# Optimization experiments

Measured on AMD Instinct MI355X. Metric: run time of the kernel, lower is better.

Reference implementation:

```python
import jax, jax.numpy as jnp
import numpy as np

B, N, C, DK, TOPK = 4, 4096, 256, 64, 8


def setup_inputs() -> dict:
    key = jax.random.key(0)
    k1, k2, k3 = jax.random.split(key, 3)
    x = jax.random.normal(k1, (B, N, C), dtype=jnp.float32)
    # nn.Linear(channels, d_k, bias=False) weights, stored as [C, DK] for x @ W
    W_q = jax.random.normal(k2, (C, DK), dtype=jnp.float32) * (C ** -0.5)
    W_k = jax.random.normal(k3, (C, DK), dtype=jnp.float32) * (C ** -0.5)
    return {"x": x, "W_q": W_q, "W_k": W_k, "top_k": TOPK}


def reference(x, W_q, W_k, top_k):
    d_k = W_q.shape[-1]
    scale = d_k ** -0.5
    Q = x @ W_q                                   # [B, N, DK]
    K = x @ W_k                                   # [B, N, DK]
    S = jnp.einsum('bnd,bmd->bnm', Q, K) * scale  # [B, N, N]
    _, topk_idx = jax.lax.top_k(S, top_k)         # [B, N, top_k]
    n = S.shape[-1]
    # scatter True at top-k column indices per row (mirrors torch scatter_)
    row_mask = lambda idx: jnp.zeros((n,), dtype=bool).at[idx].set(True)
    mask = jax.vmap(jax.vmap(row_mask))(topk_idx)  # [B, N, N] bool
    S_masked = jnp.where(mask, S, -jnp.inf)
    A = jax.nn.softmax(S_masked, axis=-1)
    return A
```

## Files before the change

kernel.cpp:

```cpp
#include <hip/hip_runtime.h>
#include <math.h>

#define NROW 16384
#define NCOL 4096
#define CDIM 256
#define DKDIM 64
#define SCALE 0.125f

typedef float v4f __attribute__((ext_vector_type(4)));

__global__ __launch_bounds__(512, 2) void qk_proj(
    const float* __restrict__ x, const float* __restrict__ Wq,
    const float* __restrict__ Wk, float* __restrict__ Qt,
    float* __restrict__ Kt) {
  __shared__ float4 xs4[64][65];
  const int t = threadIdx.x;
  const int rb = blockIdx.x;
  {
    const float4* xg = (const float4*)(x + (size_t)rb * 64 * CDIM);
    #pragma unroll
    for (int i = 0; i < 8; ++i) {
      int idx = i * 512 + t;
      xs4[idx >> 6][idx & 63] = xg[idx];
    }
  }
  __syncthreads();

  const int lane = t & 63;
  const int wu = __builtin_amdgcn_readfirstlane(t >> 6);
  const int proj = wu >> 2;
  const int chunk = wu & 3;
  const float* __restrict__ Wp = proj ? Wk : Wq;

  float acc[16];
  #pragma unroll
  for (int j = 0; j < 16; ++j) acc[j] = 0.f;

  #pragma unroll 4
  for (int cs = 0; cs < 64; ++cs) {
    float4 xv = xs4[lane][cs];
    const float xc[4] = {xv.x, xv.y, xv.z, xv.w};
    #pragma unroll
    for (int i = 0; i < 4; ++i) {
      const float4* __restrict__ w4 =
          (const float4*)(Wp + (size_t)(cs * 4 + i) * DKDIM + chunk * 16);
      float4 wa = w4[0], wb = w4[1], wc = w4[2], wd = w4[3];
      float xi = xc[i];
      acc[0]  = fmaf(xi, wa.x, acc[0]);  acc[1]  = fmaf(xi, wa.y, acc[1]);
      acc[2]  = fmaf(xi, wa.z, acc[2]);  acc[3]  = fmaf(xi, wa.w, acc[3]);
      acc[4]  = fmaf(xi, wb.x, acc[4]);  acc[5]  = fmaf(xi, wb.y, acc[5]);
      acc[6]  = fmaf(xi, wb.z, acc[6]);  acc[7]  = fmaf(xi, wb.w, acc[7]);
      acc[8]  = fmaf(xi, wc.x, acc[8]);  acc[9]  = fmaf(xi, wc.y, acc[9]);
      acc[10] = fmaf(xi, wc.z, acc[10]); acc[11] = fmaf(xi, wc.w, acc[11]);
      acc[12] = fmaf(xi, wd.x, acc[12]); acc[13] = fmaf(xi, wd.y, acc[13]);
      acc[14] = fmaf(xi, wd.z, acc[14]); acc[15] = fmaf(xi, wd.w, acc[15]);
    }
  }

  const int gr = rb * 64 + lane;
  const int b = gr >> 12;
  const int n = gr & 4095;
  float4* __restrict__ Out4 = (float4*)(proj ? Kt : Qt);
  #pragma unroll
  for (int i = 0; i < 4; ++i) {
    int dg = chunk * 4 + i;
    float4 o = {acc[4 * i], acc[4 * i + 1], acc[4 * i + 2], acc[4 * i + 3]};
    Out4[(size_t)(b * 16 + dg) * 4096 + n] = o;
  }
}

__global__ __launch_bounds__(256, 8) void s_topk(
    const float* __restrict__ Qt, const float* __restrict__ Kt,
    float* __restrict__ out, float* __restrict__ wsv, int* __restrict__ wsi) {
  __shared__ float smem[4224];
  float4* qs = (float4*)smem;
  float (*cv)[33] = (float(*)[33])smem;
  int   (*ci)[33] = (int(*)[33])(smem + 64 * 33);

  const int t = threadIdx.x;
  const int f = blockIdx.x;
  const int xs = f & 7;
  const int i5 = f >> 3;
  const int combo = xs * 4 + (i5 >> 6);
  const int rbL = i5 & 63;
  const int b = combo >> 3;
  const int chunk = combo & 7;
  const int rb = b * 64 + rbL;
  const int lane = t & 63;
  const int wu = __builtin_amdgcn_readfirstlane(t >> 6);
  const int nb = rbL * 64;

  const float4* __restrict__ Qt4 = (const float4*)Qt;
  #pragma unroll
  for (int i = 0; i < 4; ++i) {
    int idx = i * 256 + t;
    int g = idx >> 6, row = idx & 63;
    qs[g * 64 + row] = Qt4[(size_t)(b * 16 + g) * 4096 + nb + row];
  }
  __syncthreads();

  {
    v4f z = {0.f, 0.f, 0.f, 0.f};
    v4f* o4 = (v4f*)out + (size_t)rb * 64 * 1024 + chunk * 128;
    #pragma unroll 8
    for (int i = 0; i < 32; ++i) {
      int g = i * 256 + t;
      __builtin_nontemporal_store(z, &o4[(size_t)(g >> 7) * 1024 + (g & 127)]);
    }
  }

  const float4* __restrict__ Kt4 = (const float4*)Kt;
  const int stripe = chunk * 512 + wu * 128;

  float tv[8]; int ti[8]; float tmin; int tmpos;

  auto compute8 = [&](int cb, float* acc) {
    #pragma unroll
    for (int j = 0; j < 8; ++j) acc[j] = 0.f;
    #pragma unroll 2
    for (int g = 0; g < 16; ++g) {
      float4 qf = qs[g * 64 + lane];
      const float4* __restrict__ kg =
          Kt4 + (size_t)(b * 16 + g) * 4096 + cb;
      #pragma unroll
      for (int j = 0; j < 8; ++j) {
        float4 kf = kg[j];
        acc[j] = fmaf(qf.x, kf.x, acc[j]);
        acc[j] = fmaf(qf.y, kf.y, acc[j]);
        acc[j] = fmaf(qf.z, kf.z, acc[j]);
        acc[j] = fmaf(qf.w, kf.w, acc[j]);
      }
    }
  };

  {
    float acc[8];
    compute8(stripe, acc);
    #pragma unroll
    for (int j = 0; j < 8; ++j) { tv[j] = acc[j]; ti[j] = stripe + j; }
    tmin = tv[0]; tmpos = 0;
    #pragma unroll
    for (int q2 = 1; q2 < 8; ++q2)
      if (tv[q2] < tmin) { tmin = tv[q2]; tmpos = q2; }
  }

  #pragma unroll 1
  for (int cg = 1; cg < 16; ++cg) {
    const int cb = stripe + cg * 8;
    float acc[8];
    compute8(cb, acc);

    float bv = acc[0]; int bj = 0;
    #pragma unroll
    for (int j = 1; j < 8; ++j)
      if (acc[j] > bv) { bv = acc[j]; bj = j; }

    #pragma unroll
    for (int pass = 0; pass < 2; ++pass) {
      if (__any(bv > tmin)) {
        if (bv > tmin) {
          int col = cb + bj;
          #pragma unroll
          for (int q2 = 0; q2 < 8; ++q2)
            if (q2 == tmpos) { tv[q2] = bv; ti[q2] = col; }
          tmin = tv[0]; tmpos = 0;
          #pragma unroll
          for (int q2 = 1; q2 < 8; ++q2)
            if (tv[q2] < tmin) { tmin = tv[q2]; tmpos = q2; }
          #pragma unroll
          for (int j = 0; j < 8; ++j)
            if (j == bj) acc[j] = -INFINITY;
        }
        bv = acc[0]; bj = 0;
        #pragma unroll
        for (int j = 1; j < 8; ++j)
          if (acc[j] > bv) { bv = acc[j]; bj = j; }
      }
    }
    if (__any(bv > tmin)) {
      #pragma unroll
      for (int j = 0; j < 8; ++j) {
        float v = acc[j];
        if (v > tmin) {
          int col = cb + j;
          #pragma unroll
          for (int q2 = 0; q2 < 8; ++q2)
            if (q2 == tmpos) { tv[q2] = v; ti[q2] = col; }
          tmin = tv[0]; tmpos = 0;
          #pragma unroll
          for (int q2 = 1; q2 < 8; ++q2)
            if (tv[q2] < tmin) { tmin = tv[q2]; tmpos = q2; }
        }
      }
    }
  }

  __syncthreads();
  #pragma unroll
  for (int q2 = 0; q2 < 8; ++q2) {
    cv[lane][wu * 8 + q2] = tv[q2];
    ci[lane][wu * 8 + q2] = ti[q2];
  }
  __syncthreads();
  if (t < 64) {
    float rv[8]; int rid[8];
    #pragma unroll
    for (int q2 = 0; q2 < 8; ++q2) { rv[q2] = cv[t][q2]; rid[q2] = ci[t][q2]; }
    float m = rv[0]; int mp = 0;
    #pragma unroll
    for (int q2 = 1; q2 < 8; ++q2) if (rv[q2] < m) { m = rv[q2]; mp = q2; }
    #pragma unroll
    for (int c = 8; c < 32; ++c) {
      float v = cv[t][c];
      if (v > m) {
        int col = ci[t][c];
        #pragma unroll
        for (int q2 = 0; q2 < 8; ++q2) if (q2 == mp) { rv[q2] = v; rid[q2] = col; }
        m = rv[0]; mp = 0;
        #pragma unroll
        for (int q2 = 1; q2 < 8; ++q2) if (rv[q2] < m) { m = rv[q2]; mp = q2; }
      }
    }
    size_t gr = (size_t)rb * 64 + t;
    #pragma unroll
    for (int q2 = 0; q2 < 8; ++q2) {
      wsv[gr * 64 + chunk * 8 + q2] = rv[q2];
      wsi[gr * 64 + chunk * 8 + q2] = rid[q2];
    }
  }
}

__global__ __launch_bounds__(256) void merge_scatter(
    const float* __restrict__ wsv, const int* __restrict__ wsi,
    float* __restrict__ out) {
  int row = blockIdx.x * 256 + threadIdx.x;
  const float4* v4 = (const float4*)(wsv + (size_t)row * 64);
  const int4*   i4 = (const int4*)(wsi + (size_t)row * 64);
  float rv[8]; int rid[8];
  {
    float4 a0 = v4[0], a1 = v4[1];
    int4   c0 = i4[0], c1 = i4[1];
    rv[0]=a0.x; rv[1]=a0.y; rv[2]=a0.z; rv[3]=a0.w;
    rv[4]=a1.x; rv[5]=a1.y; rv[6]=a1.z; rv[7]=a1.w;
    rid[0]=c0.x; rid[1]=c0.y; rid[2]=c0.z; rid[3]=c0.w;
    rid[4]=c1.x; rid[5]=c1.y; rid[6]=c1.z; rid[7]=c1.w;
  }
  float m = rv[0]; int mp = 0;
  #pragma unroll
  for (int q = 1; q < 8; ++q) if (rv[q] < m) { m = rv[q]; mp = q; }
  #pragma unroll 2
  for (int c4 = 2; c4 < 16; ++c4) {
    float4 a = v4[c4]; int4 ic = i4[c4];
    const float vv[4] = {a.x, a.y, a.z, a.w};
    const int   ii[4] = {ic.x, ic.y, ic.z, ic.w};
    #pragma unroll
    for (int k = 0; k < 4; ++k) {
      if (vv[k] > m) {
        #pragma unroll
        for (int q = 0; q < 8; ++q) if (q == mp) { rv[q] = vv[k]; rid[q] = ii[k]; }
        m = rv[0]; mp = 0;
        #pragma unroll
        for (int q = 1; q < 8; ++q) if (rv[q] < m) { m = rv[q]; mp = q; }
      }
    }
  }
  float vmax = rv[0];
  #pragma unroll
  for (int q = 1; q < 8; ++q) vmax = fmaxf(vmax, rv[q]);
  float e[8], s = 0.f;
  #pragma unroll
  for (int q = 0; q < 8; ++q) { e[q] = __expf((rv[q] - vmax) * SCALE); s += e[q]; }
  float inv = 1.f / s;
  float* orow = out + (size_t)row * NCOL;
  #pragma unroll
  for (int q = 0; q < 8; ++q) orow[rid[q]] = e[q] * inv;
}

extern "C" void kernel_launch(void* const* d_in, const int* in_sizes, int n_in,
                              void* d_out, int out_size, void* d_ws, size_t ws_size,
                              hipStream_t stream) {
  const float* x  = (const float*)d_in[0];
  const float* Wq = (const float*)d_in[1];
  const float* Wk = (const float*)d_in[2];
  float* out = (float*)d_out;

  char* ws = (char*)d_ws;
  float* Qt  = (float*)ws;
  float* Kt  = (float*)(ws + (size_t)NROW * DKDIM * 4);
  float* wsv = (float*)(ws + 2 * (size_t)NROW * DKDIM * 4);
  int*   wsi = (int*)  (ws + 2 * (size_t)NROW * DKDIM * 4 + (size_t)NROW * 64 * 4);

  qk_proj<<<dim3(NROW / 64), 512, 0, stream>>>(x, Wq, Wk, Qt, Kt);
  s_topk<<<2048, 256, 0, stream>>>(Qt, Kt, out, wsv, wsi);
  merge_scatter<<<NROW / 256, 256, 0, stream>>>(wsv, wsi, out);
}
```

Baseline: 537.5 us.

## Process two query rows per lane in s_topk to reuse K loads

Each block now handles 128 query rows instead of 64, so every lane computes scores for two rows against the same loaded K vectors and keeps two independent top-8 lists. This halves the global/L2 K traffic per score and doubles FMA work per load. In exchange it uses more registers (launch bounds lowered to 4 blocks/CU), doubles shared memory, and halves the grid to 1024 blocks, which lowers occupancy and parallelism.

```diff
diff --git a/kernel.cpp b/kernel.cpp
--- a/kernel.cpp
+++ b/kernel.cpp
@@ -69,41 +69,41 @@
   }
 }
 
-__global__ __launch_bounds__(256, 8) void s_topk(
+__global__ __launch_bounds__(256, 4) void s_topk(
     const float* __restrict__ Qt, const float* __restrict__ Kt,
     float* __restrict__ out, float* __restrict__ wsv, int* __restrict__ wsi) {
-  __shared__ float smem[4224];
+  __shared__ float smem[8448];
   float4* qs = (float4*)smem;
   float (*cv)[33] = (float(*)[33])smem;
-  int   (*ci)[33] = (int(*)[33])(smem + 64 * 33);
+  int   (*ci)[33] = (int(*)[33])(smem + 128 * 33);
 
   const int t = threadIdx.x;
   const int f = blockIdx.x;
-  const int xs = f & 7;
+  const int slot = f & 7;
   const int i5 = f >> 3;
-  const int combo = xs * 4 + (i5 >> 6);
-  const int rbL = i5 & 63;
+  const int cl = i5 >> 5;
+  const int rbL = i5 & 31;
+  const int combo = slot * 4 + cl;
   const int b = combo >> 3;
   const int chunk = combo & 7;
-  const int rb = b * 64 + rbL;
   const int lane = t & 63;
   const int wu = __builtin_amdgcn_readfirstlane(t >> 6);
-  const int nb = rbL * 64;
+  const int n0 = rbL * 128;
 
   const float4* __restrict__ Qt4 = (const float4*)Qt;
   #pragma unroll
-  for (int i = 0; i < 4; ++i) {
+  for (int i = 0; i < 8; ++i) {
     int idx = i * 256 + t;
-    int g = idx >> 6, row = idx & 63;
-    qs[g * 64 + row] = Qt4[(size_t)(b * 16 + g) * 4096 + nb + row];
+    int g = idx >> 7, row = idx & 127;
+    qs[g * 128 + row] = Qt4[(size_t)(b * 16 + g) * 4096 + n0 + row];
   }
   __syncthreads();
 
   {
     v4f z = {0.f, 0.f, 0.f, 0.f};
-    v4f* o4 = (v4f*)out + (size_t)rb * 64 * 1024 + chunk * 128;
+    v4f* o4 = (v4f*)out + (size_t)(b * 4096 + n0) * 1024 + chunk * 128;
     #pragma unroll 8
-    for (int i = 0; i < 32; ++i) {
+    for (int i = 0; i < 64; ++i) {
       int g = i * 256 + t;
       __builtin_nontemporal_store(z, &o4[(size_t)(g >> 7) * 1024 + (g & 127)]);
     }
@@ -112,49 +112,39 @@
   const float4* __restrict__ Kt4 = (const float4*)Kt;
   const int stripe = chunk * 512 + wu * 128;
 
-  float tv[8]; int ti[8]; float tmin; int tmpos;
-
-  auto compute8 = [&](int cb, float* acc) {
-    #pragma unroll
-    for (int j = 0; j < 8; ++j) acc[j] = 0.f;
+  float tv0[8], tv1[8]; int ti0[8], ti1[8];
+  float tmin0, tmin1; int tmpos0, tmpos1;
+
+  auto compute8 = [&](int cb, float* a0, float* a1) {
+    #pragma unroll
+    for (int j = 0; j < 8; ++j) { a0[j] = 0.f; a1[j] = 0.f; }
     #pragma unroll 2
     for (int g = 0; g < 16; ++g) {
-      float4 qf = qs[g * 64 + lane];
+      float4 qa = qs[g * 128 + lane];
+      float4 qb = qs[g * 128 + 64 + lane];
       const float4* __restrict__ kg =
           Kt4 + (size_t)(b * 16 + g) * 4096 + cb;
       #pragma unroll
       for (int j = 0; j < 8; ++j) {
         float4 kf = kg[j];
-        acc[j] = fmaf(qf.x, kf.x, acc[j]);
-        acc[j] = fmaf(qf.y, kf.y, acc[j]);
-        acc[j] = fmaf(qf.z, kf.z, acc[j]);
-        acc[j] = fmaf(qf.w, kf.w, acc[j]);
+        a0[j] = fmaf(qa.x, kf.x, a0[j]);
+        a0[j] = fmaf(qa.y, kf.y, a0[j]);
+        a0[j] = fmaf(qa.z, kf.z, a0[j]);
+        a0[j] = fmaf(qa.w, kf.w, a0[j]);
+        a1[j] = fmaf(qb.x, kf.x, a1[j]);
+        a1[j] = fmaf(qb.y, kf.y, a1[j]);
+        a1[j] = fmaf(qb.z, kf.z, a1[j]);
+        a1[j] = fmaf(qb.w, kf.w, a1[j]);
       }
     }
   };
 
-  {
-    float acc[8];
-    compute8(stripe, acc);
-    #pragma unroll
-    for (int j = 0; j < 8; ++j) { tv[j] = acc[j]; ti[j] = stripe + j; }
-    tmin = tv[0]; tmpos = 0;
-    #pragma unroll
-    for (int q2 = 1; q2 < 8; ++q2)
-      if (tv[q2] < tmin) { tmin = tv[q2]; tmpos = q2; }
-  }
-
-  #pragma unroll 1
-  for (int cg = 1; cg < 16; ++cg) {
-    const int cb = stripe + cg * 8;
-    float acc[8];
-    compute8(cb, acc);
-
+  auto update8 = [&](int cb, float* acc, float* tv, int* ti,
+                     float& tmin, int& tmpos) {
     float bv = acc[0]; int bj = 0;
     #pragma unroll
     for (int j = 1; j < 8; ++j)
       if (acc[j] > bv) { bv = acc[j]; bj = j; }
-
     #pragma unroll
     for (int pass = 0; pass < 2; ++pass) {
       if (__any(bv > tmin)) {
@@ -193,16 +183,41 @@
         }
       }
     }
+  };
+
+  {
+    float a0[8], a1[8];
+    compute8(stripe, a0, a1);
+    #pragma unroll
+    for (int j = 0; j < 8; ++j) {
+      tv0[j] = a0[j]; ti0[j] = stripe + j;
+      tv1[j] = a1[j]; ti1[j] = stripe + j;
+    }
+    tmin0 = tv0[0]; tmpos0 = 0; tmin1 = tv1[0]; tmpos1 = 0;
+    #pragma unroll
+    for (int q2 = 1; q2 < 8; ++q2) {
+      if (tv0[q2] < tmin0) { tmin0 = tv0[q2]; tmpos0 = q2; }
+      if (tv1[q2] < tmin1) { tmin1 = tv1[q2]; tmpos1 = q2; }
+    }
+  }
+
+  #pragma unroll 1
+  for (int cg = 1; cg < 16; ++cg) {
+    const int cb = stripe + cg * 8;
+    float a0[8], a1[8];
+    compute8(cb, a0, a1);
+    update8(cb, a0, tv0, ti0, tmin0, tmpos0);
+    update8(cb, a1, tv1, ti1, tmin1, tmpos1);
   }
 
   __syncthreads();
   #pragma unroll
   for (int q2 = 0; q2 < 8; ++q2) {
-    cv[lane][wu * 8 + q2] = tv[q2];
-    ci[lane][wu * 8 + q2] = ti[q2];
+    cv[lane][wu * 8 + q2] = tv0[q2];       ci[lane][wu * 8 + q2] = ti0[q2];
+    cv[lane + 64][wu * 8 + q2] = tv1[q2];  ci[lane + 64][wu * 8 + q2] = ti1[q2];
   }
   __syncthreads();
-  if (t < 64) {
+  if (t < 128) {
     float rv[8]; int rid[8];
     #pragma unroll
     for (int q2 = 0; q2 < 8; ++q2) { rv[q2] = cv[t][q2]; rid[q2] = ci[t][q2]; }
@@ -221,7 +236,7 @@
         for (int q2 = 1; q2 < 8; ++q2) if (rv[q2] < m) { m = rv[q2]; mp = q2; }
       }
     }
-    size_t gr = (size_t)rb * 64 + t;
+    size_t gr = (size_t)(b * 4096 + n0) + t;
     #pragma unroll
     for (int q2 = 0; q2 < 8; ++q2) {
       wsv[gr * 64 + chunk * 8 + q2] = rv[q2];
@@ -291,6 +306,6 @@
   int*   wsi = (int*)  (ws + 2 * (size_t)NROW * DKDIM * 4 + (size_t)NROW * 64 * 4);
 
   qk_proj<<<dim3(NROW / 64), 512, 0, stream>>>(x, Wq, Wk, Qt, Kt);
-  s_topk<<<2048, 256, 0, stream>>>(Qt, Kt, out, wsv, wsi);
+  s_topk<<<1024, 256, 0, stream>>>(Qt, Kt, out, wsv, wsi);
   merge_scatter<<<NROW / 256, 256, 0, stream>>>(wsv, wsi, out);
 }
```

New measurement: 546.8 us. No clear change (+1.7%).

## Tile K layout into 8-column blocks, software-pipeline K loads, defer zero-fill stores

Applied to the files above, without the earlier changes.

The K projection is now written in a blocked layout: for each group of 8 columns, all 16 d-groups of 8 float4s sit contiguously, so each column-group's K tile is one 2KB contiguous read. The score loop is hand-unrolled with double-buffered register loads, so the next d-group loads while the current one's FMAs run. The zero-fill of the output is moved after the top-k search so stores no longer compete with the K loads. The top-k initialization is unified via -inf, and launch bounds are relaxed to 4 blocks per SM to allow more registers, at the cost of occupancy.

```diff
diff --git a/kernel.cpp b/kernel.cpp
--- a/kernel.cpp
+++ b/kernel.cpp
@@ -60,16 +60,26 @@
   const int gr = rb * 64 + lane;
   const int b = gr >> 12;
   const int n = gr & 4095;
-  float4* __restrict__ Out4 = (float4*)(proj ? Kt : Qt);
-  #pragma unroll
-  for (int i = 0; i < 4; ++i) {
-    int dg = chunk * 4 + i;
-    float4 o = {acc[4 * i], acc[4 * i + 1], acc[4 * i + 2], acc[4 * i + 3]};
-    Out4[(size_t)(b * 16 + dg) * 4096 + n] = o;
+  if (proj == 0) {
+    float4* __restrict__ Out4 = (float4*)Qt;
+    #pragma unroll
+    for (int i = 0; i < 4; ++i) {
+      int dg = chunk * 4 + i;
+      float4 o = {acc[4 * i], acc[4 * i + 1], acc[4 * i + 2], acc[4 * i + 3]};
+      Out4[(size_t)(b * 16 + dg) * 4096 + n] = o;
+    }
+  } else {
+    float4* __restrict__ Out4 = (float4*)Kt;
+    #pragma unroll
+    for (int i = 0; i < 4; ++i) {
+      int dg = chunk * 4 + i;
+      float4 o = {acc[4 * i], acc[4 * i + 1], acc[4 * i + 2], acc[4 * i + 3]};
+      Out4[(((size_t)b * 512 + (n >> 3)) * 16 + dg) * 8 + (n & 7)] = o;
+    }
   }
 }
 
-__global__ __launch_bounds__(256, 8) void s_topk(
+__global__ __launch_bounds__(256, 4) void s_topk(
     const float* __restrict__ Qt, const float* __restrict__ Kt,
     float* __restrict__ out, float* __restrict__ wsv, int* __restrict__ wsi) {
   __shared__ float smem[4224];
@@ -79,9 +89,9 @@
 
   const int t = threadIdx.x;
   const int f = blockIdx.x;
-  const int xs = f & 7;
+  const int slot = f & 7;
   const int i5 = f >> 3;
-  const int combo = xs * 4 + (i5 >> 6);
+  const int combo = slot * 4 + (i5 >> 6);
   const int rbL = i5 & 63;
   const int b = combo >> 3;
   const int chunk = combo & 7;
@@ -99,62 +109,66 @@
   }
   __syncthreads();
 
-  {
-    v4f z = {0.f, 0.f, 0.f, 0.f};
-    v4f* o4 = (v4f*)out + (size_t)rb * 64 * 1024 + chunk * 128;
-    #pragma unroll 8
-    for (int i = 0; i < 32; ++i) {
-      int g = i * 256 + t;
-      __builtin_nontemporal_store(z, &o4[(size_t)(g >> 7) * 1024 + (g & 127)]);
-    }
-  }
-
   const float4* __restrict__ Kt4 = (const float4*)Kt;
   const int stripe = chunk * 512 + wu * 128;
-
-  float tv[8]; int ti[8]; float tmin; int tmpos;
-
-  auto compute8 = [&](int cb, float* acc) {
+  const float4* __restrict__ Kb =
+      Kt4 + ((size_t)b * 512 + chunk * 64 + wu * 16) * 128;
+
+  float tv[8]; int ti[8]; float tmin = -INFINITY; int tmpos = 0;
+  #pragma unroll
+  for (int q2 = 0; q2 < 8; ++q2) { tv[q2] = -INFINITY; ti[q2] = 0; }
+
+#define LOADG_(P0,P1,P2,P3,P4,P5,P6,P7, gg) \
+  { const float4* __restrict__ pp = pc + (gg) * 8; \
+    P0 = pp[0]; P1 = pp[1]; P2 = pp[2]; P3 = pp[3]; \
+    P4 = pp[4]; P5 = pp[5]; P6 = pp[6]; P7 = pp[7]; }
+#define LOADG(L, gg) LOADG_(L, gg)
+
+#define FMA1(KF, j) \
+  acc[j] = fmaf(qa.x, KF.x, acc[j]); acc[j] = fmaf(qa.y, KF.y, acc[j]); \
+  acc[j] = fmaf(qa.z, KF.z, acc[j]); acc[j] = fmaf(qa.w, KF.w, acc[j]);
+
+#define FMAG_(P0,P1,P2,P3,P4,P5,P6,P7, gg) \
+  { float4 qa = qs[(gg) * 64 + lane]; \
+    FMA1(P0, 0) FMA1(P1, 1) FMA1(P2, 2) FMA1(P3, 3) \
+    FMA1(P4, 4) FMA1(P5, 5) FMA1(P6, 6) FMA1(P7, 7) }
+#define FMAG(L, gg) FMAG_(L, gg)
+
+#define LA KA0,KA1,KA2,KA3,KA4,KA5,KA6,KA7
+#define LB KB0,KB1,KB2,KB3,KB4,KB5,KB6,KB7
+
+  #pragma unroll 1
+  for (int cg = 0; cg < 16; ++cg) {
+    const int cb = stripe + cg * 8;
+    const float4* __restrict__ pc = Kb + (size_t)cg * 128;
+    float acc[8];
     #pragma unroll
     for (int j = 0; j < 8; ++j) acc[j] = 0.f;
-    #pragma unroll 2
-    for (int g = 0; g < 16; ++g) {
-      float4 qf = qs[g * 64 + lane];
-      const float4* __restrict__ kg =
-          Kt4 + (size_t)(b * 16 + g) * 4096 + cb;
-      #pragma unroll
-      for (int j = 0; j < 8; ++j) {
-        float4 kf = kg[j];
-        acc[j] = fmaf(qf.x, kf.x, acc[j]);
-        acc[j] = fmaf(qf.y, kf.y, acc[j]);
-        acc[j] = fmaf(qf.z, kf.z, acc[j]);
-        acc[j] = fmaf(qf.w, kf.w, acc[j]);
-      }
-    }
-  };
-
-  {
-    float acc[8];
-    compute8(stripe, acc);
-    #pragma unroll
-    for (int j = 0; j < 8; ++j) { tv[j] = acc[j]; ti[j] = stripe + j; }
-    tmin = tv[0]; tmpos = 0;
-    #pragma unroll
-    for (int q2 = 1; q2 < 8; ++q2)
-      if (tv[q2] < tmin) { tmin = tv[q2]; tmpos = q2; }
-  }
-
-  #pragma unroll 1
-  for (int cg = 1; cg < 16; ++cg) {
-    const int cb = stripe + cg * 8;
-    float acc[8];
-    compute8(cb, acc);
+
+    float4 KA0,KA1,KA2,KA3,KA4,KA5,KA6,KA7;
+    float4 KB0,KB1,KB2,KB3,KB4,KB5,KB6,KB7;
+    LOADG(LA, 0)
+    LOADG(LB, 1)  FMAG(LA, 0)
+    LOADG(LA, 2)  FMAG(LB, 1)
+    LOADG(LB, 3)  FMAG(LA, 2)
+    LOADG(LA, 4)  FMAG(LB, 3)
+    LOADG(LB, 5)  FMAG(LA, 4)
+    LOADG(LA, 6)  FMAG(LB, 5)
+    LOADG(LB, 7)  FMAG(LA, 6)
+    LOADG(LA, 8)  FMAG(LB, 7)
+    LOADG(LB, 9)  FMAG(LA, 8)
+    LOADG(LA, 10) FMAG(LB, 9)
+    LOADG(LB, 11) FMAG(LA, 10)
+    LOADG(LA, 12) FMAG(LB, 11)
+    LOADG(LB, 13) FMAG(LA, 12)
+    LOADG(LA, 14) FMAG(LB, 13)
+    LOADG(LB, 15) FMAG(LA, 14)
+    FMAG(LB, 15)
 
     float bv = acc[0]; int bj = 0;
     #pragma unroll
     for (int j = 1; j < 8; ++j)
       if (acc[j] > bv) { bv = acc[j]; bj = j; }
-
     #pragma unroll
     for (int pass = 0; pass < 2; ++pass) {
       if (__any(bv > tmin)) {
@@ -192,6 +206,16 @@
             if (tv[q2] < tmin) { tmin = tv[q2]; tmpos = q2; }
         }
       }
+    }
+  }
+
+  {
+    v4f z = {0.f, 0.f, 0.f, 0.f};
+    v4f* o4 = (v4f*)out + (size_t)rb * 64 * 1024 + chunk * 128;
+    #pragma unroll 4
+    for (int i = 0; i < 32; ++i) {
+      int g = i * 256 + t;
+      __builtin_nontemporal_store(z, &o4[(size_t)(g >> 7) * 1024 + (g & 127)]);
     }
   }
 
```

Measured after the change: 632.5 us. +17.7%, slower.
